# Performance work log

Hardware: AMD Instinct MI355X
Metric: run time of the kernel (lower is better)

Reference implementation:

```python
import jax, jax.numpy as jnp
import numpy as np

B = 65536
H = 256
STEPS = 128


def setup_inputs() -> dict:
    key = jax.random.key(0)
    ks = jax.random.split(key, 6)
    scale = 0.1
    return {
        "x": jax.random.normal(ks[0], (B, H), dtype=jnp.float32),
        "W_hh": jax.random.normal(ks[1], (H, H), dtype=jnp.float32) * scale,
        "fc1_w": jax.random.normal(ks[2], (H, H), dtype=jnp.float32) * (1.0 / np.sqrt(H)),
        "fc1_b": jax.random.normal(ks[3], (H,), dtype=jnp.float32) * 0.01,
        "fc2_w": jax.random.normal(ks[4], (H, H), dtype=jnp.float32) * (1.0 / np.sqrt(H)),
        "fc2_b": jax.random.normal(ks[5], (H,), dtype=jnp.float32) * 0.01,
        "steps": STEPS,
    }


def reference(x, W_hh, fc1_w, fc1_b, fc2_w, fc2_b, steps):
    # h = fc1(x)  (torch Linear: x @ W.T + b)
    h0 = x @ fc1_w.T + fc1_b

    def step(h, _):
        return jnp.tanh(h @ W_hh), None

    h, _ = jax.lax.scan(step, h0, None, length=steps)
    out = h @ fc2_w.T + fc2_b
    return (out, h)
```

## Files before the change

### kernel.cpp

```cpp
#include <hip/hip_runtime.h>
#include <math.h>

#define Hd 256
#define BM 128
#define KP 16
#define NP 16
#define THREADS 512
#define HLD 64
#define WLD 256

__device__ __forceinline__ float tanh_xla(float x) {
    const float plus_clamp = 7.90531110763549805f;
    float xc = fminf(fmaxf(x, -plus_clamp), plus_clamp);
    float x2 = xc * xc;
    float p = fmaf(x2, -2.76076847742355e-16f, 2.00018790482477e-13f);
    p = fmaf(x2, p, -8.60467152213735e-11f);
    p = fmaf(x2, p,  5.12229709037114e-08f);
    p = fmaf(x2, p,  1.48572235717979e-05f);
    p = fmaf(x2, p,  6.37261928875436e-04f);
    p = fmaf(x2, p,  4.89352455891786e-03f);
    p = xc * p;
    float q = fmaf(x2, 1.19825839466702e-06f, 1.18534705686654e-04f);
    q = fmaf(x2, q, 2.26843463243900e-03f);
    q = fmaf(x2, q, 4.89352518554385e-03f);
    float r = p / q;
    return (fabsf(x) < 0.0004f) ? x : r;
}

__global__ __launch_bounds__(THREADS, 1)
void rnn_fused(const float* __restrict__ x, const float* __restrict__ Whh,
               const float* __restrict__ fc1w, const float* __restrict__ fc1b,
               const float* __restrict__ fc2w, const float* __restrict__ fc2b,
               float* __restrict__ outF, float* __restrict__ hF) {
    __shared__ __align__(16) float Hs0[Hd][HLD];
    __shared__ __align__(16) float Hs1[Hd][HLD];
    __shared__ __align__(16) float Wp[2][KP][WLD];

    const int  t    = threadIdx.x;
    const long row0 = (long)blockIdx.x * BM;
    const int  tm   = t & 15;
    const int  tn   = t >> 4;

    {
        const int r  = t >> 2;
        const int kq = (t & 3) * 4;
        float (*H)[HLD] = (r < 64) ? Hs0 : Hs1;
        const int m = r & 63;
        const float* src = x + (row0 + r) * Hd + kq;
#pragma unroll
        for (int q = 0; q < 16; ++q) {
            float4 v = *reinterpret_cast<const float4*>(src + q * 16);
            const int k = q * 16 + kq;
            H[k + 0][m] = v.x;
            H[k + 1][m] = v.y;
            H[k + 2][m] = v.z;
            H[k + 3][m] = v.w;
        }
    }

    float accL[4][8], accH[4][8];
    float4 pf0, pf1;

    auto ld_nt = [&](const float* W, int p) {
        const float4* b4 = reinterpret_cast<const float4*>(W + (long)p * KP * Hd);
        pf0 = b4[t];
        pf1 = b4[THREADS + t];
    };
    auto st_nt = [&](int buf) {
        float4* d4 = reinterpret_cast<float4*>(&Wp[buf][0][0]);
        d4[t]           = pf0;
        d4[THREADS + t] = pf1;
    };
    auto ld_t = [&](const float* W, int p) {
        const int k0 = p * KP;
        int n0 = t >> 1;           int kq0 = (t & 1) * 8;
        pf0 = *reinterpret_cast<const float4*>(W + (long)n0 * Hd + k0 + kq0);
        pf1 = *reinterpret_cast<const float4*>(W + (long)n0 * Hd + k0 + kq0 + 4);
    };
    auto st_t = [&](int buf) {
        int n0 = t >> 1;           int kq0 = (t & 1) * 8;
        const float* f0 = reinterpret_cast<const float*>(&pf0);
        const float* f1 = reinterpret_cast<const float*>(&pf1);
#pragma unroll
        for (int i = 0; i < 4; ++i) Wp[buf][kq0 + i][n0]     = f0[i];
#pragma unroll
        for (int i = 0; i < 4; ++i) Wp[buf][kq0 + 4 + i][n0] = f1[i];
    };

    auto zero_acc = [&]() {
#pragma unroll
        for (int i = 0; i < 4; ++i)
#pragma unroll
            for (int j = 0; j < 8; ++j) { accL[i][j] = 0.f; accH[i][j] = 0.f; }
    };

    auto compute_panel = [&](int buf, int kbase) {
#pragma unroll 2
        for (int kk = 0; kk < KP; ++kk) {
            float4 aL = *reinterpret_cast<const float4*>(&Hs0[kbase + kk][tm * 4]);
            float4 aH = *reinterpret_cast<const float4*>(&Hs1[kbase + kk][tm * 4]);
            float4 w0 = *reinterpret_cast<const float4*>(&Wp[buf][kk][tn * 8]);
            float4 w1 = *reinterpret_cast<const float4*>(&Wp[buf][kk][tn * 8 + 4]);
            const float al[4] = {aL.x, aL.y, aL.z, aL.w};
            const float ah[4] = {aH.x, aH.y, aH.z, aH.w};
            const float ww[8] = {w0.x, w0.y, w0.z, w0.w, w1.x, w1.y, w1.z, w1.w};
#pragma unroll
            for (int i = 0; i < 4; ++i)
#pragma unroll
                for (int j = 0; j < 8; ++j) {
                    accL[i][j] = fmaf(al[i], ww[j], accL[i][j]);
                    accH[i][j] = fmaf(ah[i], ww[j], accH[i][j]);
                }
        }
    };

    auto run_nt = [&](const float* W) {
        zero_acc();
#pragma unroll 1
        for (int p = 0; p < NP; ++p) {
            ld_nt(W, (p + 1) & 15);
            compute_panel(p & 1, p * KP);
            st_nt((p + 1) & 1);
            __syncthreads();
        }
    };
    auto run_t = [&](const float* W) {
        zero_acc();
#pragma unroll 1
        for (int p = 0; p < NP; ++p) {
            ld_t(W, (p + 1) & 15);
            compute_panel(p & 1, p * KP);
            st_t((p + 1) & 1);
            __syncthreads();
        }
    };

    auto writeback_h = [&]() {
#pragma unroll
        for (int j = 0; j < 8; ++j) {
            *reinterpret_cast<float4*>(&Hs0[tn * 8 + j][tm * 4]) =
                make_float4(accL[0][j], accL[1][j], accL[2][j], accL[3][j]);
            *reinterpret_cast<float4*>(&Hs1[tn * 8 + j][tm * 4]) =
                make_float4(accH[0][j], accH[1][j], accH[2][j], accH[3][j]);
        }
    };

    ld_t(fc1w, 0); st_t(0);
    __syncthreads();
    run_t(fc1w);
    {
        float4 b0 = *reinterpret_cast<const float4*>(fc1b + tn * 8);
        float4 b1 = *reinterpret_cast<const float4*>(fc1b + tn * 8 + 4);
        const float bj[8] = {b0.x, b0.y, b0.z, b0.w, b1.x, b1.y, b1.z, b1.w};
#pragma unroll
        for (int i = 0; i < 4; ++i)
#pragma unroll
            for (int j = 0; j < 8; ++j) { accL[i][j] += bj[j]; accH[i][j] += bj[j]; }
    }
    writeback_h();
    __syncthreads();

    ld_nt(Whh, 0); st_nt(0);
    __syncthreads();
#pragma unroll 1
    for (int s = 0; s < 128; ++s) {
        run_nt(Whh);
#pragma unroll
        for (int i = 0; i < 4; ++i)
#pragma unroll
            for (int j = 0; j < 8; ++j) {
                accL[i][j] = tanh_xla(accL[i][j]);
                accH[i][j] = tanh_xla(accH[i][j]);
            }
        writeback_h();
        __syncthreads();
    }

#pragma unroll
    for (int i = 0; i < 4; ++i) {
        const long rL = row0 + tm * 4 + i;
        const long rH = rL + 64;
        *reinterpret_cast<float4*>(&hF[rL * Hd + tn * 8]) =
            make_float4(accL[i][0], accL[i][1], accL[i][2], accL[i][3]);
        *reinterpret_cast<float4*>(&hF[rL * Hd + tn * 8 + 4]) =
            make_float4(accL[i][4], accL[i][5], accL[i][6], accL[i][7]);
        *reinterpret_cast<float4*>(&hF[rH * Hd + tn * 8]) =
            make_float4(accH[i][0], accH[i][1], accH[i][2], accH[i][3]);
        *reinterpret_cast<float4*>(&hF[rH * Hd + tn * 8 + 4]) =
            make_float4(accH[i][4], accH[i][5], accH[i][6], accH[i][7]);
    }

    ld_t(fc2w, 0); st_t(0);
    __syncthreads();
    run_t(fc2w);
    {
        float4 b0 = *reinterpret_cast<const float4*>(fc2b + tn * 8);
        float4 b1 = *reinterpret_cast<const float4*>(fc2b + tn * 8 + 4);
        const float bj[8] = {b0.x, b0.y, b0.z, b0.w, b1.x, b1.y, b1.z, b1.w};
#pragma unroll
        for (int i = 0; i < 4; ++i)
#pragma unroll
            for (int j = 0; j < 8; ++j) { accL[i][j] += bj[j]; accH[i][j] += bj[j]; }
    }
#pragma unroll
    for (int i = 0; i < 4; ++i) {
        const long rL = row0 + tm * 4 + i;
        const long rH = rL + 64;
        *reinterpret_cast<float4*>(&outF[rL * Hd + tn * 8]) =
            make_float4(accL[i][0], accL[i][1], accL[i][2], accL[i][3]);
        *reinterpret_cast<float4*>(&outF[rL * Hd + tn * 8 + 4]) =
            make_float4(accL[i][4], accL[i][5], accL[i][6], accL[i][7]);
        *reinterpret_cast<float4*>(&outF[rH * Hd + tn * 8]) =
            make_float4(accH[i][0], accH[i][1], accH[i][2], accH[i][3]);
        *reinterpret_cast<float4*>(&outF[rH * Hd + tn * 8 + 4]) =
            make_float4(accH[i][4], accH[i][5], accH[i][6], accH[i][7]);
    }
}

extern "C" void kernel_launch(void* const* d_in, const int* in_sizes, int n_in,
                              void* d_out, int out_size, void* d_ws, size_t ws_size,
                              hipStream_t stream) {
    const float* x     = (const float*)d_in[0];
    const float* W_hh  = (const float*)d_in[1];
    const float* fc1_w = (const float*)d_in[2];
    const float* fc1_b = (const float*)d_in[3];
    const float* fc2_w = (const float*)d_in[4];
    const float* fc2_b = (const float*)d_in[5];

    const int B = in_sizes[0] / Hd;
    float* out = (float*)d_out;
    float* h   = out + (long)B * Hd;

    rnn_fused<<<dim3(B / BM), dim3(THREADS), 0, stream>>>(
        x, W_hh, fc1_w, fc1_b, fc2_w, fc2_b, out, h);
}
```

Measured before the change: 13.08 ms.

## Read W_hh directly from global/L1 in recurrent loop instead of LDS panels

The recurrent steps no longer stage W_hh panels through shared memory with double buffering and per-panel barriers. Each thread now loads its 8 weight columns straight from global memory (expected to hit cache) for all 256 k values. This cuts the 16 barriers per step down to two and removes LDS store traffic. The cost is a global/L1 load of two float4s on every k iteration, with latency that is no longer hidden by the software prefetch.

```diff
diff --git a/kernel.cpp b/kernel.cpp
--- a/kernel.cpp
+++ b/kernel.cpp
@@ -61,16 +61,6 @@
     float accL[4][8], accH[4][8];
     float4 pf0, pf1;
 
-    auto ld_nt = [&](const float* W, int p) {
-        const float4* b4 = reinterpret_cast<const float4*>(W + (long)p * KP * Hd);
-        pf0 = b4[t];
-        pf1 = b4[THREADS + t];
-    };
-    auto st_nt = [&](int buf) {
-        float4* d4 = reinterpret_cast<float4*>(&Wp[buf][0][0]);
-        d4[t]           = pf0;
-        d4[THREADS + t] = pf1;
-    };
     auto ld_t = [&](const float* W, int p) {
         const int k0 = p * KP;
         int n0 = t >> 1;           int kq0 = (t & 1) * 8;
@@ -92,6 +82,16 @@
         for (int i = 0; i < 4; ++i)
 #pragma unroll
             for (int j = 0; j < 8; ++j) { accL[i][j] = 0.f; accH[i][j] = 0.f; }
+    };
+
+    auto fma_block = [&](const float al[4], const float ah[4], const float ww[8]) {
+#pragma unroll
+        for (int i = 0; i < 4; ++i)
+#pragma unroll
+            for (int j = 0; j < 8; ++j) {
+                accL[i][j] = fmaf(al[i], ww[j], accL[i][j]);
+                accH[i][j] = fmaf(ah[i], ww[j], accH[i][j]);
+            }
     };
 
     auto compute_panel = [&](int buf, int kbase) {
@@ -104,26 +104,10 @@
             const float al[4] = {aL.x, aL.y, aL.z, aL.w};
             const float ah[4] = {aH.x, aH.y, aH.z, aH.w};
             const float ww[8] = {w0.x, w0.y, w0.z, w0.w, w1.x, w1.y, w1.z, w1.w};
-#pragma unroll
-            for (int i = 0; i < 4; ++i)
-#pragma unroll
-                for (int j = 0; j < 8; ++j) {
-                    accL[i][j] = fmaf(al[i], ww[j], accL[i][j]);
-                    accH[i][j] = fmaf(ah[i], ww[j], accH[i][j]);
-                }
-        }
-    };
-
-    auto run_nt = [&](const float* W) {
-        zero_acc();
-#pragma unroll 1
-        for (int p = 0; p < NP; ++p) {
-            ld_nt(W, (p + 1) & 15);
-            compute_panel(p & 1, p * KP);
-            st_nt((p + 1) & 1);
-            __syncthreads();
-        }
-    };
+            fma_block(al, ah, ww);
+        }
+    };
+
     auto run_t = [&](const float* W) {
         zero_acc();
 #pragma unroll 1
@@ -160,11 +144,22 @@
     writeback_h();
     __syncthreads();
 
-    ld_nt(Whh, 0); st_nt(0);
-    __syncthreads();
+    const float* Wbase = Whh + tn * 8;
 #pragma unroll 1
     for (int s = 0; s < 128; ++s) {
-        run_nt(Whh);
+        zero_acc();
+#pragma unroll 2
+        for (int k = 0; k < Hd; ++k) {
+            float4 aL = *reinterpret_cast<const float4*>(&Hs0[k][tm * 4]);
+            float4 aH = *reinterpret_cast<const float4*>(&Hs1[k][tm * 4]);
+            const float* wr = Wbase + (long)k * Hd;
+            float4 w0 = *reinterpret_cast<const float4*>(wr);
+            float4 w1 = *reinterpret_cast<const float4*>(wr + 4);
+            const float al[4] = {aL.x, aL.y, aL.z, aL.w};
+            const float ah[4] = {aH.x, aH.y, aH.z, aH.w};
+            const float ww[8] = {w0.x, w0.y, w0.z, w0.w, w1.x, w1.y, w1.z, w1.w};
+            fma_block(al, ah, ww);
+        }
 #pragma unroll
         for (int i = 0; i < 4; ++i)
 #pragma unroll
@@ -172,6 +167,7 @@
                 accL[i][j] = tanh_xla(accL[i][j]);
                 accH[i][j] = tanh_xla(accH[i][j]);
             }
+        __syncthreads();
         writeback_h();
         __syncthreads();
     }
```

Measured after the change: 13.35 ms. 1.02x slower.
